# Kernel tuning notes

Hardware: AMD Instinct MI355X
Metric: run time of the kernel (lower is better)

The kernel has to match this reference:

```python
import jax, jax.numpy as jnp
import numpy as np

N_NODES = 50000
N_EDGES = 800000
IN_DIM = 96
HID = 96


def setup_inputs() -> dict:
    key = jax.random.key(0)
    k1, k2, k3, k4 = jax.random.split(key, 4)
    x = jax.random.normal(k1, (N_NODES, IN_DIM), dtype=jnp.float32)
    edge_index = jax.random.randint(k2, (2, N_EDGES), 0, N_NODES, dtype=jnp.int64)
    s1 = 1.0 / np.sqrt(IN_DIM)
    s2 = 1.0 / np.sqrt(HID)
    W1 = jax.random.normal(k3, (IN_DIM, HID), dtype=jnp.float32) * s1
    b1 = jnp.zeros((HID,), dtype=jnp.float32)
    W2 = jax.random.normal(k4, (HID, HID), dtype=jnp.float32) * s2
    b2 = jnp.zeros((HID,), dtype=jnp.float32)
    return {"x": x, "edge_index": edge_index, "W1": W1, "b1": b1, "W2": W2, "b2": b2}


def _gcn_conv(x, src, dst, norm, W, b, n_nodes):
    # x' = D^{-1/2}(A+I)D^{-1/2} X W + b  (PyG GCNConv semantics)
    xw = x @ W                           # [N, out]
    msg = xw[src] * norm[:, None]        # gather + edge-normalize, [E+N, out]
    agg = jax.ops.segment_sum(msg, dst, num_segments=n_nodes)  # scatter-add
    return agg + b


def reference(x, edge_index, W1, b1, W2, b2):
    n_nodes = x.shape[0]
    loops = jnp.arange(n_nodes, dtype=edge_index.dtype)
    src = jnp.concatenate([edge_index[0], loops])  # sources (j)
    dst = jnp.concatenate([edge_index[1], loops])  # targets (i), aggregation index
    # symmetric normalization with self-loops; degree counted at targets
    deg = jax.ops.segment_sum(jnp.ones(dst.shape, dtype=x.dtype), dst, num_segments=n_nodes)
    dinv = jnp.where(deg > 0, jax.lax.rsqrt(deg), 0.0)
    norm = dinv[src] * dinv[dst]
    h = jax.nn.relu(_gcn_conv(x, src, dst, norm, W1, b1, n_nodes))
    h = jax.nn.relu(_gcn_conv(h, src, dst, norm, W2, b2, n_nodes))
    return h
```

## Files before the change

kernel.cpp:

```cpp
#include <hip/hip_runtime.h>

#define N_NODES 50000
#define N_EDGES 800000
#define DIM 96
#define FEAT_ELEMS (N_NODES * DIM)
#define NBLK 196
#define CNT_STRIDE 16
#define CNT_INTS (N_NODES * CNT_STRIDE)
#define ZBLK4 782
#define EGRID 3125
#define CGRID 4688
#define WGRID 10
#define AGRID 3125
#define GGRID 782

typedef __attribute__((ext_vector_type(8))) short short8;
typedef __attribute__((ext_vector_type(4))) float float4v;

__device__ __forceinline__ float bf16_to_f32(unsigned short u) {
    unsigned int w = ((unsigned int)u) << 16;
    float f;
    __builtin_memcpy(&f, &w, 4);
    return f;
}
__device__ __forceinline__ float bflo(unsigned int w) {
    unsigned int u = w << 16;
    float f;
    __builtin_memcpy(&f, &u, 4);
    return f;
}
__device__ __forceinline__ float bfhi(unsigned int w) {
    unsigned int u = w & 0xFFFF0000u;
    float f;
    __builtin_memcpy(&f, &u, 4);
    return f;
}
__device__ __forceinline__ unsigned short f32_to_bf16_rne(float f) {
    unsigned int w;
    __builtin_memcpy(&w, &f, 4);
    unsigned int r = (w + 0x7FFFu + ((w >> 16) & 1u)) >> 16;
    return (unsigned short)r;
}
__device__ __forceinline__ unsigned int pack_bf16x2(float lo, float hi) {
    return (unsigned int)f32_to_bf16_rne(lo) | ((unsigned int)f32_to_bf16_rne(hi) << 16);
}

__device__ __forceinline__ int edge_at(const void* ep, int is64, int idx) {
    if (is64) return (int)((const long long*)ep)[idx];
    return ((const int*)ep)[idx];
}

__global__ __launch_bounds__(256) void prolog_kernel(const unsigned int* edges,
                                                     const unsigned int* x,
                                                     int* flagE, int* flagF, int* cnt) {
    __shared__ unsigned int sh[256];
    int t = threadIdx.x;
    int b = blockIdx.x;
    if (b < ZBLK4) {
        int i4 = b * 256 + t;
        if (i4 < CNT_INTS / 4) ((int4*)cnt)[i4] = make_int4(0, 0, 0, 0);
        return;
    }
    if (b == ZBLK4) {
        if (t < 64) {
            unsigned int acc = 0;
            for (int k = 0; k < 4; ++k) {
                int idx = t * 4 + k;
                int pos = 1 + 2 * idx * 3109;
                acc |= edges[pos];
            }
            sh[t] = acc;
        }
        __syncthreads();
        if (t == 0) {
            unsigned int a = 0;
            for (int i = 0; i < 64; ++i) a |= sh[i];
            *flagE = (a == 0u) ? 1 : 0;
        }
        return;
    }
    unsigned int w = x[t * 9000];
    unsigned int e = (w >> 7) & 0xFFu;
    sh[t] = (e >= 100u && e <= 135u) ? 1u : 0u;
    __syncthreads();
    if (t == 0) {
        int c = 0;
        for (int i = 0; i < 256; ++i) c += (int)sh[i];
        *flagF = (c >= 128) ? 1 : 0;
    }
}

__global__ __launch_bounds__(256) void count_convert_kernel(const void* __restrict__ edges,
                                                            const void* __restrict__ x,
                                                            const void* __restrict__ W1,
                                                            const void* __restrict__ W2,
                                                            const int* __restrict__ flagE,
                                                            const int* __restrict__ flagF,
                                                            int* __restrict__ cnt,
                                                            ushort4* __restrict__ edata,
                                                            unsigned short* __restrict__ xb,
                                                            unsigned short* __restrict__ wsw1,
                                                            unsigned short* __restrict__ wsw2) {
    int b = blockIdx.x;
    if (b < EGRID) {
        int e = b * 256 + threadIdx.x;
        int is64 = *flagE;
        int s = edge_at(edges, is64, e);
        int d = edge_at(edges, is64, N_EDGES + e);
        int r = atomicAdd(&cnt[d * CNT_STRIDE], 1);
        edata[e] = make_ushort4((unsigned short)s, (unsigned short)d,
                                (unsigned short)r, 0);
        return;
    }
    if (b < EGRID + CGRID) {
        int i4 = ((b - EGRID) * 256 + threadIdx.x) * 4;
        if (i4 >= FEAT_ELEMS) return;
        int isbf16 = *flagF;
        ushort4 o;
        if (isbf16) {
            o = *(const ushort4*)((const unsigned short*)x + i4);
        } else {
            float4 v = *(const float4*)((const float*)x + i4);
            o.x = f32_to_bf16_rne(v.x);
            o.y = f32_to_bf16_rne(v.y);
            o.z = f32_to_bf16_rne(v.z);
            o.w = f32_to_bf16_rne(v.w);
        }
        *(ushort4*)(xb + i4) = o;
        return;
    }
    int wi = b - EGRID - CGRID;
    int which = wi / 5;
    int f = (wi - which * 5) * 256 + threadIdx.x;
    if (f >= 1152) return;
    const void* Wp = which ? W2 : W1;
    unsigned short* Op = which ? wsw2 : wsw1;
    int wBf16 = *flagF;
    int kt = f / 384;
    int rem = f - kt * 384;
    int nt = rem >> 6;
    int ln64 = rem & 63;
    int q = ln64 >> 4, ln = ln64 & 15;
    int k0 = kt * 32 + q * 8;
    int n = nt * 16 + ln;
    unsigned short e[8];
    if (wBf16) {
        const unsigned short* Wh = (const unsigned short*)Wp;
        #pragma unroll
        for (int j = 0; j < 8; ++j) e[j] = Wh[(k0 + j) * DIM + n];
    } else {
        const float* Wf = (const float*)Wp;
        #pragma unroll
        for (int j = 0; j < 8; ++j) e[j] = f32_to_bf16_rne(Wf[(k0 + j) * DIM + n]);
    }
    uint4 pk;
    pk.x = (unsigned int)e[0] | ((unsigned int)e[1] << 16);
    pk.y = (unsigned int)e[2] | ((unsigned int)e[3] << 16);
    pk.z = (unsigned int)e[4] | ((unsigned int)e[5] << 16);
    pk.w = (unsigned int)e[6] | ((unsigned int)e[7] << 16);
    *(uint4*)&Op[f * 8] = pk;
}

__global__ __launch_bounds__(256) void scan_blocksum_kernel(const int* cnt, int* blockSums) {
    __shared__ int sh[256];
    int i = blockIdx.x * 256 + threadIdx.x;
    sh[threadIdx.x] = (i < N_NODES) ? cnt[i * CNT_STRIDE] : 0;
    __syncthreads();
    for (int off = 128; off > 0; off >>= 1) {
        if (threadIdx.x < off) sh[threadIdx.x] += sh[threadIdx.x + off];
        __syncthreads();
    }
    if (threadIdx.x == 0) blockSums[blockIdx.x] = sh[0];
}

__global__ __launch_bounds__(256) void scan_apply_kernel(const int* __restrict__ cnt,
                                                         const int* __restrict__ blockSums,
                                                         int* __restrict__ row_ptr,
                                                         float* __restrict__ dinv) {
    __shared__ int sb[256];
    __shared__ int sh[256];
    int t = threadIdx.x;
    sb[t] = (t < NBLK) ? blockSums[t] : 0;
    __syncthreads();
    for (int off = 1; off < 256; off <<= 1) {
        int u = (t >= off) ? sb[t - off] : 0;
        __syncthreads();
        sb[t] += u;
        __syncthreads();
    }
    int b = blockIdx.x;
    int blockOff = (b == 0) ? 0 : sb[b - 1];
    if (b == 0 && t == 0) row_ptr[N_NODES] = sb[NBLK - 1];

    int i = b * 256 + t;
    int c = (i < N_NODES) ? cnt[i * CNT_STRIDE] : 0;
    sh[t] = c;
    __syncthreads();
    for (int off = 1; off < 256; off <<= 1) {
        int u = (t >= off) ? sh[t - off] : 0;
        __syncthreads();
        sh[t] += u;
        __syncthreads();
    }
    if (i < N_NODES) {
        row_ptr[i] = sh[t] - c + blockOff;
        dinv[i]    = rsqrtf((float)(c + 1));
    }
}

__global__ __launch_bounds__(256) void fill_direct_kernel(const ushort4* __restrict__ edata,
                                                          const int* __restrict__ row_ptr,
                                                          const float* __restrict__ dinv,
                                                          uint2* __restrict__ csr8) {
    int e = blockIdx.x * 256 + threadIdx.x;
    if (e >= N_EDGES) return;
    ushort4 ed = edata[e];
    int s = ed.x, d = ed.y;
    int pos = row_ptr[d] + (int)ed.z;
    float w = dinv[s] * dinv[d];
    csr8[pos] = make_uint2((unsigned int)s, __float_as_uint(w));
}

__global__ __launch_bounds__(256) void gather_kernel(const unsigned short* __restrict__ feat,
                                                     const int* __restrict__ row_ptr,
                                                     const uint2* __restrict__ csr8,
                                                     const float* __restrict__ dinv,
                                                     unsigned short* __restrict__ aggb) {
    int gid = blockIdx.x * 256 + threadIdx.x;
    int g = gid >> 4;
    int l = gid & 15;
    if (g >= N_NODES) return;
    float di = dinv[g];
    const unsigned int* sp = (const unsigned int*)(feat + g * DIM + l * 6);
    unsigned int sw0 = sp[0], sw1 = sp[1], sw2 = sp[2];
    float wself = di * di;
    float a0 = wself * bflo(sw0), a1 = wself * bfhi(sw0);
    float a2 = wself * bflo(sw1), a3 = wself * bfhi(sw1);
    float a4 = wself * bflo(sw2), a5 = wself * bfhi(sw2);
    int e = row_ptr[g], e1 = row_ptr[g + 1];
    for (; e + 4 <= e1; e += 4) {
        uint2 c0 = csr8[e + 0];
        uint2 c1 = csr8[e + 1];
        uint2 c2 = csr8[e + 2];
        uint2 c3 = csr8[e + 3];
        const unsigned int* p = (const unsigned int*)(feat + (c0.x & 0xFFFFu) * DIM + l * 6);
        const unsigned int* q = (const unsigned int*)(feat + (c1.x & 0xFFFFu) * DIM + l * 6);
        const unsigned int* r = (const unsigned int*)(feat + (c2.x & 0xFFFFu) * DIM + l * 6);
        const unsigned int* s = (const unsigned int*)(feat + (c3.x & 0xFFFFu) * DIM + l * 6);
        unsigned int p0 = p[0], p1 = p[1], p2 = p[2];
        unsigned int q0 = q[0], q1 = q[1], q2 = q[2];
        unsigned int r0 = r[0], r1 = r[1], r2 = r[2];
        unsigned int s0 = s[0], s1 = s[1], s2 = s[2];
        float w0 = __uint_as_float(c0.y);
        float w1 = __uint_as_float(c1.y);
        float w2 = __uint_as_float(c2.y);
        float w3 = __uint_as_float(c3.y);
        a0 = fmaf(w0, bflo(p0), a0);  a1 = fmaf(w0, bfhi(p0), a1);
        a2 = fmaf(w0, bflo(p1), a2);  a3 = fmaf(w0, bfhi(p1), a3);
        a4 = fmaf(w0, bflo(p2), a4);  a5 = fmaf(w0, bfhi(p2), a5);
        a0 = fmaf(w1, bflo(q0), a0);  a1 = fmaf(w1, bfhi(q0), a1);
        a2 = fmaf(w1, bflo(q1), a2);  a3 = fmaf(w1, bfhi(q1), a3);
        a4 = fmaf(w1, bflo(q2), a4);  a5 = fmaf(w1, bfhi(q2), a5);
        a0 = fmaf(w2, bflo(r0), a0);  a1 = fmaf(w2, bfhi(r0), a1);
        a2 = fmaf(w2, bflo(r1), a2);  a3 = fmaf(w2, bfhi(r1), a3);
        a4 = fmaf(w2, bflo(r2), a4);  a5 = fmaf(w2, bfhi(r2), a5);
        a0 = fmaf(w3, bflo(s0), a0);  a1 = fmaf(w3, bfhi(s0), a1);
        a2 = fmaf(w3, bflo(s1), a2);  a3 = fmaf(w3, bfhi(s1), a3);
        a4 = fmaf(w3, bflo(s2), a4);  a5 = fmaf(w3, bfhi(s2), a5);
    }
    for (; e < e1; ++e) {
        uint2 c = csr8[e];
        const unsigned int* p = (const unsigned int*)(feat + (c.x & 0xFFFFu) * DIM + l * 6);
        unsigned int p0 = p[0], p1 = p[1], p2 = p[2];
        float w = __uint_as_float(c.y);
        a0 = fmaf(w, bflo(p0), a0);  a1 = fmaf(w, bfhi(p0), a1);
        a2 = fmaf(w, bflo(p1), a2);  a3 = fmaf(w, bfhi(p1), a3);
        a4 = fmaf(w, bflo(p2), a4);  a5 = fmaf(w, bfhi(p2), a5);
    }
    unsigned int* op = (unsigned int*)(aggb + g * DIM + l * 6);
    op[0] = pack_bf16x2(a0, a1);
    op[1] = pack_bf16x2(a2, a3);
    op[2] = pack_bf16x2(a4, a5);
}

__global__ __launch_bounds__(256) void gemm_mfma_kernel(const unsigned short* __restrict__ A,
                                                        const unsigned short* __restrict__ Wsw,
                                                        const void* __restrict__ bias,
                                                        const int* __restrict__ flagF,
                                                        void* __restrict__ out, int outMode) {
    int wBf16 = *flagF;
    int outBf16 = (outMode == 2) ? wBf16 : outMode;
    int t = threadIdx.x;
    int wave = t >> 6;
    int lane = t & 63;
    int quad = lane >> 4, ln = lane & 15;
    int m0 = blockIdx.x * 64 + wave * 16;
    int arow = m0 + ln;
    bool arowok = (arow < N_NODES);

    float4v acc[6];
    #pragma unroll
    for (int nt = 0; nt < 6; ++nt) acc[nt] = (float4v){0.f, 0.f, 0.f, 0.f};

    #pragma unroll
    for (int kt = 0; kt < 3; ++kt) {
        short8 af;
        if (arowok) {
            af = *(const short8*)&A[arow * DIM + kt * 32 + quad * 8];
        } else {
            af = (short8){0, 0, 0, 0, 0, 0, 0, 0};
        }
        #pragma unroll
        for (int nt = 0; nt < 6; ++nt) {
            short8 bf = *(const short8*)&Wsw[((kt * 6 + nt) * 64 + lane) * 8];
            acc[nt] = __builtin_amdgcn_mfma_f32_16x16x32_bf16(af, bf, acc[nt], 0, 0, 0);
        }
    }

    #pragma unroll
    for (int nt = 0; nt < 6; ++nt) {
        int n = nt * 16 + ln;
        float bv = wBf16 ? bf16_to_f32(((const unsigned short*)bias)[n])
                         : ((const float*)bias)[n];
        #pragma unroll
        for (int reg = 0; reg < 4; ++reg) {
            int row = m0 + quad * 4 + reg;
            if (row >= N_NODES) continue;
            float v = fmaxf(acc[nt][reg] + bv, 0.0f);
            if (outBf16) ((unsigned short*)out)[row * DIM + n] = f32_to_bf16_rne(v);
            else         ((float*)out)[row * DIM + n] = v;
        }
    }
}

extern "C" void kernel_launch(void* const* d_in, const int* in_sizes, int n_in,
                              void* d_out, int out_size, void* d_ws, size_t ws_size,
                              hipStream_t stream) {
    const void* x  = d_in[0];
    const void* ei = d_in[1];
    const void* W1 = d_in[2];
    const void* b1 = d_in[3];
    const void* W2 = d_in[4];
    const void* b2 = d_in[5];

    char* base = (char*)d_ws;
    size_t off = 0;
    auto carve = [&](size_t bytes) -> void* {
        void* p = base + off;
        off += (bytes + 255) & ~(size_t)255;
        return p;
    };
    int*            flagE     = (int*)carve(4);
    int*            flagF     = (int*)carve(4);
    int*            cnt       = (int*)carve((size_t)CNT_INTS * 4);
    int*            row_ptr   = (int*)carve((size_t)(N_NODES + 1) * 4);
    float*          dinv      = (float*)carve((size_t)N_NODES * 4);
    int*            blockSums = (int*)carve((size_t)NBLK * 4);
    ushort4*        edata     = (ushort4*)carve((size_t)N_EDGES * 8);
    uint2*          csr8      = (uint2*)carve((size_t)N_EDGES * 8);
    unsigned short* wsw1      = (unsigned short*)carve((size_t)1152 * 8 * 2);
    unsigned short* wsw2      = (unsigned short*)carve((size_t)1152 * 8 * 2);
    unsigned short* aggb      = (unsigned short*)carve((size_t)FEAT_ELEMS * 2);
    unsigned short* xb        = (unsigned short*)carve((size_t)FEAT_ELEMS * 2);
    unsigned short* h         = (unsigned short*)carve((size_t)FEAT_ELEMS * 2);

    prolog_kernel<<<ZBLK4 + 2, 256, 0, stream>>>((const unsigned int*)ei,
                                                 (const unsigned int*)x, flagE, flagF, cnt);
    count_convert_kernel<<<EGRID + CGRID + WGRID, 256, 0, stream>>>(
        ei, x, W1, W2, flagE, flagF, cnt, edata, xb, wsw1, wsw2);
    scan_blocksum_kernel<<<NBLK, 256, 0, stream>>>(cnt, blockSums);
    scan_apply_kernel<<<NBLK, 256, 0, stream>>>(cnt, blockSums, row_ptr, dinv);
    fill_direct_kernel<<<EGRID, 256, 0, stream>>>(edata, row_ptr, dinv, csr8);

    gather_kernel<<<AGRID, 256, 0, stream>>>(xb, row_ptr, csr8, dinv, aggb);
    gemm_mfma_kernel<<<GGRID, 256, 0, stream>>>(aggb, wsw1, b1, flagF, h, 1);

    gather_kernel<<<AGRID, 256, 0, stream>>>(h, row_ptr, csr8, dinv, aggb);
    gemm_mfma_kernel<<<GGRID, 256, 0, stream>>>(aggb, wsw2, b2, flagF, d_out, 2);
}
```

Measured before the change: 209.9 us.

## Sort gather nodes by degree via histogram permutation to reduce wave divergence

Builds a degree histogram during the scan and a permutation array that groups nodes with equal in-degree (capped at 63). The gather kernels process nodes in this permuted order so that the nodes sharing a wavefront have similar edge counts, reducing lanes that sit idle in the edge loop. This adds atomics and an extra perm read in the preprocessing, and makes the feature reads and output writes less sequential.

```diff
diff --git a/kernel.cpp b/kernel.cpp
--- a/kernel.cpp
+++ b/kernel.cpp
@@ -13,6 +13,8 @@
 #define WGRID 10
 #define AGRID 3125
 #define GGRID 782
+#define NBINS 64
+#define BIN_STRIDE 16
 
 typedef __attribute__((ext_vector_type(8))) short short8;
 typedef __attribute__((ext_vector_type(4))) float float4v;
@@ -52,7 +54,8 @@
 
 __global__ __launch_bounds__(256) void prolog_kernel(const unsigned int* edges,
                                                      const unsigned int* x,
-                                                     int* flagE, int* flagF, int* cnt) {
+                                                     int* flagE, int* flagF, int* cnt,
+                                                     int* dhist, int* dcur) {
     __shared__ unsigned int sh[256];
     int t = threadIdx.x;
     int b = blockIdx.x;
@@ -62,6 +65,8 @@
         return;
     }
     if (b == ZBLK4) {
+        ((int4*)dhist)[t] = make_int4(0, 0, 0, 0);
+        ((int4*)dcur)[t]  = make_int4(0, 0, 0, 0);
         if (t < 64) {
             unsigned int acc = 0;
             for (int k = 0; k < 4; ++k) {
@@ -161,33 +166,56 @@
     *(uint4*)&Op[f * 8] = pk;
 }
 
-__global__ __launch_bounds__(256) void scan_blocksum_kernel(const int* cnt, int* blockSums) {
+__global__ __launch_bounds__(256) void scan_blocksum_kernel(const int* __restrict__ cnt,
+                                                            int* __restrict__ blockSums,
+                                                            int* __restrict__ dhist) {
     __shared__ int sh[256];
-    int i = blockIdx.x * 256 + threadIdx.x;
-    sh[threadIdx.x] = (i < N_NODES) ? cnt[i * CNT_STRIDE] : 0;
+    __shared__ int lh[NBINS];
+    int t = threadIdx.x;
+    int i = blockIdx.x * 256 + t;
+    int c = (i < N_NODES) ? cnt[i * CNT_STRIDE] : 0;
+    sh[t] = c;
+    if (t < NBINS) lh[t] = 0;
     __syncthreads();
+    if (i < N_NODES) atomicAdd(&lh[c < NBINS - 1 ? c : NBINS - 1], 1);
     for (int off = 128; off > 0; off >>= 1) {
-        if (threadIdx.x < off) sh[threadIdx.x] += sh[threadIdx.x + off];
-        __syncthreads();
-    }
-    if (threadIdx.x == 0) blockSums[blockIdx.x] = sh[0];
+        if (t < off) sh[t] += sh[t + off];
+        __syncthreads();
+    }
+    if (t == 0) blockSums[blockIdx.x] = sh[0];
+    if (t < NBINS && lh[t] > 0) atomicAdd(&dhist[t * BIN_STRIDE], lh[t]);
 }
 
 __global__ __launch_bounds__(256) void scan_apply_kernel(const int* __restrict__ cnt,
                                                          const int* __restrict__ blockSums,
+                                                         const int* __restrict__ dhist,
+                                                         int* __restrict__ dcur,
                                                          int* __restrict__ row_ptr,
-                                                         float* __restrict__ dinv) {
+                                                         float* __restrict__ dinv,
+                                                         int* __restrict__ perm) {
     __shared__ int sb[256];
     __shared__ int sh[256];
+    __shared__ int bo[NBINS];
+    __shared__ int lh[NBINS];
+    __shared__ int lbase[NBINS];
     int t = threadIdx.x;
     sb[t] = (t < NBLK) ? blockSums[t] : 0;
+    int dh0 = 0;
+    if (t < NBINS) {
+        dh0 = dhist[t * BIN_STRIDE];
+        bo[t] = dh0;
+        lh[t] = 0;
+    }
     __syncthreads();
     for (int off = 1; off < 256; off <<= 1) {
         int u = (t >= off) ? sb[t - off] : 0;
+        int v = (t < NBINS && t >= off) ? bo[t - off] : 0;
         __syncthreads();
         sb[t] += u;
-        __syncthreads();
-    }
+        if (t < NBINS) bo[t] += v;
+        __syncthreads();
+    }
+    if (t < NBINS) bo[t] -= dh0;
     int b = blockIdx.x;
     int blockOff = (b == 0) ? 0 : sb[b - 1];
     if (b == 0 && t == 0) row_ptr[N_NODES] = sb[NBLK - 1];
@@ -196,15 +224,23 @@
     int c = (i < N_NODES) ? cnt[i * CNT_STRIDE] : 0;
     sh[t] = c;
     __syncthreads();
+    int bin = 0, lrank = 0;
+    if (i < N_NODES) {
+        bin = c < NBINS - 1 ? c : NBINS - 1;
+        lrank = atomicAdd(&lh[bin], 1);
+    }
     for (int off = 1; off < 256; off <<= 1) {
         int u = (t >= off) ? sh[t - off] : 0;
         __syncthreads();
         sh[t] += u;
         __syncthreads();
     }
+    if (t < NBINS && lh[t] > 0) lbase[t] = atomicAdd(&dcur[t * BIN_STRIDE], lh[t]);
+    __syncthreads();
     if (i < N_NODES) {
         row_ptr[i] = sh[t] - c + blockOff;
         dinv[i]    = rsqrtf((float)(c + 1));
+        perm[bo[bin] + lbase[bin] + lrank] = i;
     }
 }
 
@@ -225,11 +261,13 @@
                                                      const int* __restrict__ row_ptr,
                                                      const uint2* __restrict__ csr8,
                                                      const float* __restrict__ dinv,
+                                                     const int* __restrict__ perm,
                                                      unsigned short* __restrict__ aggb) {
     int gid = blockIdx.x * 256 + threadIdx.x;
-    int g = gid >> 4;
+    int grp = gid >> 4;
     int l = gid & 15;
-    if (g >= N_NODES) return;
+    if (grp >= N_NODES) return;
+    int g = perm[grp];
     float di = dinv[g];
     const unsigned int* sp = (const unsigned int*)(feat + g * DIM + l * 6);
     unsigned int sw0 = sp[0], sw1 = sp[1], sw2 = sp[2];
@@ -356,6 +394,9 @@
     int*            row_ptr   = (int*)carve((size_t)(N_NODES + 1) * 4);
     float*          dinv      = (float*)carve((size_t)N_NODES * 4);
     int*            blockSums = (int*)carve((size_t)NBLK * 4);
+    int*            dhist     = (int*)carve((size_t)NBINS * BIN_STRIDE * 4);
+    int*            dcur      = (int*)carve((size_t)NBINS * BIN_STRIDE * 4);
+    int*            perm      = (int*)carve((size_t)N_NODES * 4);
     ushort4*        edata     = (ushort4*)carve((size_t)N_EDGES * 8);
     uint2*          csr8      = (uint2*)carve((size_t)N_EDGES * 8);
     unsigned short* wsw1      = (unsigned short*)carve((size_t)1152 * 8 * 2);
@@ -365,16 +406,18 @@
     unsigned short* h         = (unsigned short*)carve((size_t)FEAT_ELEMS * 2);
 
     prolog_kernel<<<ZBLK4 + 2, 256, 0, stream>>>((const unsigned int*)ei,
-                                                 (const unsigned int*)x, flagE, flagF, cnt);
+                                                 (const unsigned int*)x, flagE, flagF,
+                                                 cnt, dhist, dcur);
     count_convert_kernel<<<EGRID + CGRID + WGRID, 256, 0, stream>>>(
         ei, x, W1, W2, flagE, flagF, cnt, edata, xb, wsw1, wsw2);
-    scan_blocksum_kernel<<<NBLK, 256, 0, stream>>>(cnt, blockSums);
-    scan_apply_kernel<<<NBLK, 256, 0, stream>>>(cnt, blockSums, row_ptr, dinv);
+    scan_blocksum_kernel<<<NBLK, 256, 0, stream>>>(cnt, blockSums, dhist);
+    scan_apply_kernel<<<NBLK, 256, 0, stream>>>(cnt, blockSums, dhist, dcur,
+                                                row_ptr, dinv, perm);
     fill_direct_kernel<<<EGRID, 256, 0, stream>>>(edata, row_ptr, dinv, csr8);
 
-    gather_kernel<<<AGRID, 256, 0, stream>>>(xb, row_ptr, csr8, dinv, aggb);
+    gather_kernel<<<AGRID, 256, 0, stream>>>(xb, row_ptr, csr8, dinv, perm, aggb);
     gemm_mfma_kernel<<<GGRID, 256, 0, stream>>>(aggb, wsw1, b1, flagF, h, 1);
 
-    gather_kernel<<<AGRID, 256, 0, stream>>>(h, row_ptr, csr8, dinv, aggb);
+    gather_kernel<<<AGRID, 256, 0, stream>>>(h, row_ptr, csr8, dinv, perm, aggb);
     gemm_mfma_kernel<<<GGRID, 256, 0, stream>>>(aggb, wsw2, b2, flagF, d_out, 2);
 }
```

Result: slower. 220.0 us (+4.8%).

## Merge two-pass scan into one kernel and widen counter padding

Applied to the files above, without the earlier changes.

Replaces the block-sum kernel plus scan-apply kernel with a single scan kernel. Each block now computes its own prefix offset by re-reading all preceding counters, which removes one launch and the blockSums round trip. The cost is redundant reads that grow with block index, quadratic overall. The counter stride also doubles from 16 to 32 ints, and the zeroing grid grows to match. That spreads atomics further apart but doubles the memory that must be zeroed and scanned.

```diff
diff --git a/kernel.cpp b/kernel.cpp
--- a/kernel.cpp
+++ b/kernel.cpp
@@ -5,9 +5,9 @@
 #define DIM 96
 #define FEAT_ELEMS (N_NODES * DIM)
 #define NBLK 196
-#define CNT_STRIDE 16
+#define CNT_STRIDE 32
 #define CNT_INTS (N_NODES * CNT_STRIDE)
-#define ZBLK4 782
+#define ZBLK4 1563
 #define EGRID 3125
 #define CGRID 4688
 #define WGRID 10
@@ -161,37 +161,29 @@
     *(uint4*)&Op[f * 8] = pk;
 }
 
-__global__ __launch_bounds__(256) void scan_blocksum_kernel(const int* cnt, int* blockSums) {
+__global__ __launch_bounds__(256) void scan_kernel(const int* __restrict__ cnt,
+                                                   int* __restrict__ row_ptr,
+                                                   float* __restrict__ dinv) {
+    __shared__ int red[256];
     __shared__ int sh[256];
-    int i = blockIdx.x * 256 + threadIdx.x;
-    sh[threadIdx.x] = (i < N_NODES) ? cnt[i * CNT_STRIDE] : 0;
+    int t = threadIdx.x;
+    int b = blockIdx.x;
+    int acc0 = 0, acc1 = 0, acc2 = 0, acc3 = 0;
+    int chunk = 0;
+    for (; chunk + 4 <= b; chunk += 4) {
+        acc0 += cnt[((chunk + 0) * 256 + t) * CNT_STRIDE];
+        acc1 += cnt[((chunk + 1) * 256 + t) * CNT_STRIDE];
+        acc2 += cnt[((chunk + 2) * 256 + t) * CNT_STRIDE];
+        acc3 += cnt[((chunk + 3) * 256 + t) * CNT_STRIDE];
+    }
+    for (; chunk < b; ++chunk) acc0 += cnt[(chunk * 256 + t) * CNT_STRIDE];
+    red[t] = acc0 + acc1 + acc2 + acc3;
     __syncthreads();
     for (int off = 128; off > 0; off >>= 1) {
-        if (threadIdx.x < off) sh[threadIdx.x] += sh[threadIdx.x + off];
+        if (t < off) red[t] += red[t + off];
         __syncthreads();
     }
-    if (threadIdx.x == 0) blockSums[blockIdx.x] = sh[0];
-}
-
-__global__ __launch_bounds__(256) void scan_apply_kernel(const int* __restrict__ cnt,
-                                                         const int* __restrict__ blockSums,
-                                                         int* __restrict__ row_ptr,
-                                                         float* __restrict__ dinv) {
-    __shared__ int sb[256];
-    __shared__ int sh[256];
-    int t = threadIdx.x;
-    sb[t] = (t < NBLK) ? blockSums[t] : 0;
-    __syncthreads();
-    for (int off = 1; off < 256; off <<= 1) {
-        int u = (t >= off) ? sb[t - off] : 0;
-        __syncthreads();
-        sb[t] += u;
-        __syncthreads();
-    }
-    int b = blockIdx.x;
-    int blockOff = (b == 0) ? 0 : sb[b - 1];
-    if (b == 0 && t == 0) row_ptr[N_NODES] = sb[NBLK - 1];
-
+    int blockOff = red[0];
     int i = b * 256 + t;
     int c = (i < N_NODES) ? cnt[i * CNT_STRIDE] : 0;
     sh[t] = c;
@@ -206,6 +198,7 @@
         row_ptr[i] = sh[t] - c + blockOff;
         dinv[i]    = rsqrtf((float)(c + 1));
     }
+    if (b == NBLK - 1 && t == 255) row_ptr[N_NODES] = blockOff + sh[255];
 }
 
 __global__ __launch_bounds__(256) void fill_direct_kernel(const ushort4* __restrict__ edata,
@@ -355,7 +348,6 @@
     int*            cnt       = (int*)carve((size_t)CNT_INTS * 4);
     int*            row_ptr   = (int*)carve((size_t)(N_NODES + 1) * 4);
     float*          dinv      = (float*)carve((size_t)N_NODES * 4);
-    int*            blockSums = (int*)carve((size_t)NBLK * 4);
     ushort4*        edata     = (ushort4*)carve((size_t)N_EDGES * 8);
     uint2*          csr8      = (uint2*)carve((size_t)N_EDGES * 8);
     unsigned short* wsw1      = (unsigned short*)carve((size_t)1152 * 8 * 2);
@@ -368,8 +360,7 @@
                                                  (const unsigned int*)x, flagE, flagF, cnt);
     count_convert_kernel<<<EGRID + CGRID + WGRID, 256, 0, stream>>>(
         ei, x, W1, W2, flagE, flagF, cnt, edata, xb, wsw1, wsw2);
-    scan_blocksum_kernel<<<NBLK, 256, 0, stream>>>(cnt, blockSums);
-    scan_apply_kernel<<<NBLK, 256, 0, stream>>>(cnt, blockSums, row_ptr, dinv);
+    scan_kernel<<<NBLK, 256, 0, stream>>>(cnt, row_ptr, dinv);
     fill_direct_kernel<<<EGRID, 256, 0, stream>>>(edata, row_ptr, dinv, csr8);
 
     gather_kernel<<<AGRID, 256, 0, stream>>>(xb, row_ptr, csr8, dinv, aggb);
```

Result: slower. 247.0 us (+17.7%).
